# Performance work log

Hardware: AMD Instinct MI355X
Metric: run time of the kernel (lower is better)

Reference implementation:

```python
import jax, jax.numpy as jnp
import numpy as np

T, H, I = 8192, 4096, 11008  # tokens, hidden, intermediate (LLaMA-7B)


def setup_inputs() -> dict:
    key = jax.random.key(0)
    ks = jax.random.split(key, 8)
    # int8-valued tensors stored as int32 (spec dtype enum lacks int8)
    hidden_states = jax.random.randint(ks[0], (T, H), -128, 128, dtype=jnp.int32)
    gate_w = jax.random.randint(ks[1], (I, H), -128, 128, dtype=jnp.int32)
    up_w = jax.random.randint(ks[2], (I, H), -128, 128, dtype=jnp.int32)
    down_w = jax.random.randint(ks[3], (H, I), -128, 128, dtype=jnp.int32)
    # per-tensor dequant scales (alpha = input_scale * weight_scale); small so
    # the SwiGLU product lands roughly in int8 range before requantization
    gate_a = jnp.float32(0.004)
    up_a = jnp.float32(0.004)
    down_a = jnp.float32(0.004)
    gate_b = jax.random.normal(ks[4], (I,), dtype=jnp.float32)
    up_b = jax.random.normal(ks[5], (I,), dtype=jnp.float32)
    down_b = jax.random.normal(ks[6], (H,), dtype=jnp.float32)
    return dict(hidden_states=hidden_states, gate_w=gate_w, gate_a=gate_a,
                gate_b=gate_b, up_w=up_w, up_a=up_a, up_b=up_b,
                down_w=down_w, down_a=down_a, down_b=down_b)


def _w8a8_linear(x_i8, w_i8, alpha, bias):
    # scale alpha and fp32 bias (W8A8BFP32OFP32Linear semantics).
    acc = jnp.matmul(x_i8.astype(jnp.int8), w_i8.astype(jnp.int8).T,
                     preferred_element_type=jnp.int32)
    return acc.astype(jnp.float32) * alpha + bias


def reference(hidden_states, gate_w, gate_a, gate_b, up_w, up_a, up_b,
              down_w, down_a, down_b):
    x1 = jax.nn.silu(_w8a8_linear(hidden_states, gate_w, gate_a, gate_b))  # [T,I]
    x2 = _w8a8_linear(hidden_states, up_w, up_a, up_b)                     # [T,I]
    x = x1 * x2
    # requantize: round, clamp to int8 range
    q = jnp.clip(jnp.round(x), -128.0, 127.0).astype(jnp.int32)
    return _w8a8_linear(q, down_w, down_a, down_b)                          # [T,H]
```

## Files before the change

### kernel.cpp

```cpp
#include <hip/hip_runtime.h>
#include <math.h>

#define T_DIM 8192
#define H_DIM 4096
#define I_DIM 11008

typedef int v4i  __attribute__((ext_vector_type(4)));
typedef int v16i __attribute__((ext_vector_type(16)));

#define MFMA8 __builtin_amdgcn_mfma_i32_32x32x32_i8

#define AS1(p) ((const __attribute__((address_space(1))) void*)(p))
#define AS3(p) ((__attribute__((address_space(3))) void*)(p))

#define WAIT_VM_BAR(N) asm volatile("s_waitcnt vmcnt(" #N ")\n\ts_barrier" ::: "memory")
#define LGKM(N) do { asm volatile("s_waitcnt lgkmcnt(" #N ")" ::: "memory"); \
                     __builtin_amdgcn_sched_barrier(0); } while (0)

__device__ __forceinline__ v4i DSR(const char* p) {
  v4i r;
  unsigned a = (unsigned)(size_t)(const __attribute__((address_space(3))) char*)p;
  asm volatile("ds_read_b128 %0, %1" : "=v"(r) : "v"(a));
  return r;
}

#define STG(buf, src, soff, doff) \
  __builtin_amdgcn_global_load_lds(AS1((src) + (soff)), AS3((buf) + (doff) + dd), 16, 0, 0)

__global__ void pack_shuf(const int* __restrict__ src, char* __restrict__ dst,
                          int nk32, long nchunk) {
  long c = (long)blockIdx.x * blockDim.x + threadIdx.x;
  long stride = (long)gridDim.x * blockDim.x;
  for (; c < nchunk; c += stride) {
    int lane = (int)(c & 63);
    long rk = c >> 6;
    long r32 = rk / nk32;
    int k32 = (int)(rk - r32 * nk32);
    const int4* s = (const int4*)(src + (r32 * 32 + (lane & 31)) * (long)(nk32 * 32)
                                      + (long)k32 * 32 + ((lane >> 5) << 4));
    int4 a = s[0], b = s[1], cc = s[2], d = s[3];
    int w0 = (a.x & 255) | ((a.y & 255) << 8) | ((a.z & 255) << 16) | (a.w << 24);
    int w1 = (b.x & 255) | ((b.y & 255) << 8) | ((b.z & 255) << 16) | (b.w << 24);
    int w2 = (cc.x & 255) | ((cc.y & 255) << 8) | ((cc.z & 255) << 16) | (cc.w << 24);
    int w3 = (d.x & 255) | ((d.y & 255) << 8) | ((d.z & 255) << 16) | (d.w << 24);
    ((int4*)dst)[c] = make_int4(w0, w1, w2, w3);
  }
}

__global__ __launch_bounds__(512, 2) void gemm_gateup(
    const char* __restrict__ A, const char* __restrict__ Bg, const char* __restrict__ Bu,
    const float* __restrict__ ga_p, const float* __restrict__ gb,
    const float* __restrict__ ua_p, const float* __restrict__ ub,
    char* __restrict__ Q)
{
  __shared__ char lds[2][65536];
  const int tid = threadIdx.x;
  const int l = tid & 63;
  const int w = tid >> 6;
  const int wm = w >> 2, wn = w & 3;
  const int li32 = l & 31, kg2 = l >> 5;

  const int q8 = 2752 / 8;
  int bid = blockIdx.x;
  int wgid = (bid & 7) * q8 + (bid >> 3);
  int st = wgid >> 3, r = wgid & 7;
  int sm = st / 43, sn = st - sm * 43;
  const int m0 = (sm * 4 + (r & 3)) * 256;
  const int n0 = (sn * 2 + (r >> 2)) * 128;

  const int NK = H_DIM / 32;
  const int NT = H_DIM / 128;

  v16i accg[4], accu[4];
#pragma unroll
  for (int i = 0; i < 4; ++i) {
#pragma unroll
    for (int j = 0; j < 16; ++j) { accg[i][j] = 0; accu[i][j] = 0; }
  }

  const char* pA = A + ((size_t)((m0 >> 5) + (tid >> 6)) * NK << 10) + ((tid & 63) << 4);
  const char* pB = (tid < 256)
      ? Bg + ((size_t)((n0 >> 5) + (tid >> 6)) * NK << 10) + ((tid & 63) << 4)
      : Bu + ((size_t)((n0 >> 5) + ((tid >> 6) - 4)) * NK << 10) + ((tid & 63) << 4);
  const int dd = tid * 16;

  const int oA0 = (wm * 4 + 0) * 1024 + l * 16;
  const int oA1 = (wm * 4 + 1) * 1024 + l * 16;
  const int oA2 = (wm * 4 + 2) * 1024 + l * 16;
  const int oA3 = (wm * 4 + 3) * 1024 + l * 16;
  const int oG  = 8192  + wn * 1024 + l * 16;
  const int oU  = 12288 + wn * 1024 + l * 16;

  v4i E0, E1, E2, E3, Eg, Eu;
  v4i O0, O1, O2, O3, Og, Ou;

#define RD_GU(S, B, soff)                                                 \
  do {                                                                    \
    S##0 = DSR((B) + (soff) + oA0); S##1 = DSR((B) + (soff) + oA1);       \
    S##2 = DSR((B) + (soff) + oA2); S##3 = DSR((B) + (soff) + oA3);       \
    S##g = DSR((B) + (soff) + oG);  S##u = DSR((B) + (soff) + oU);        \
  } while (0)

#define MM_GU(S)                                                          \
  do {                                                                    \
    __builtin_amdgcn_s_setprio(1);                                        \
    accg[0] = MFMA8(S##0, S##g, accg[0], 0, 0, 0);                        \
    accu[0] = MFMA8(S##0, S##u, accu[0], 0, 0, 0);                        \
    accg[1] = MFMA8(S##1, S##g, accg[1], 0, 0, 0);                        \
    accu[1] = MFMA8(S##1, S##u, accu[1], 0, 0, 0);                        \
    accg[2] = MFMA8(S##2, S##g, accg[2], 0, 0, 0);                        \
    accu[2] = MFMA8(S##2, S##u, accu[2], 0, 0, 0);                        \
    accg[3] = MFMA8(S##3, S##g, accg[3], 0, 0, 0);                        \
    accu[3] = MFMA8(S##3, S##u, accu[3], 0, 0, 0);                        \
    __builtin_amdgcn_s_setprio(0);                                        \
  } while (0)

  {
    char* B0 = lds[0];
    STG(B0, pA, 0,    0);     STG(B0, pA, 1024, 16384);
    STG(B0, pA, 2048, 32768); STG(B0, pA, 3072, 49152);
    STG(B0, pB, 0,    8192);  STG(B0, pB, 1024, 24576);
    STG(B0, pB, 2048, 40960); STG(B0, pB, 3072, 57344);
    WAIT_VM_BAR(0);
    RD_GU(E, B0, 0);
  }

  for (int t = 0; t < NT; ++t) {
    char* L  = lds[t & 1];
    char* SB = lds[(t & 1) ^ 1];
    const bool son = (t + 1) < NT;
    const long sk = (long)(t + 1) * 4096;

    RD_GU(O, L, 16384);
    if (son) { STG(SB, pA, sk, 0);            STG(SB, pA, sk + 1024, 16384);
               STG(SB, pA, sk + 2048, 32768); STG(SB, pA, sk + 3072, 49152); }
    LGKM(6);
    MM_GU(E);
    RD_GU(E, L, 32768);
    if (son) { STG(SB, pB, sk, 8192);         STG(SB, pB, sk + 1024, 24576);
               STG(SB, pB, sk + 2048, 40960); STG(SB, pB, sk + 3072, 57344); }
    LGKM(6);
    MM_GU(O);
    RD_GU(O, L, 49152);
    LGKM(6);
    MM_GU(E);
    LGKM(0);
    MM_GU(O);
    __builtin_amdgcn_sched_barrier(0);
    WAIT_VM_BAR(0);
    if (son) RD_GU(E, SB, 0);
  }
#undef RD_GU
#undef MM_GU

  const float ga = *ga_p, ua = *ua_p;
  const int col = n0 + wn * 32 + li32;
  const float gbv = gb[col], ubv = ub[col];
  const int k32q = (n0 >> 5) + wn;
  const int lanehi = ((li32 >> 4) & 1) << 5;
  const int bytelo = li32 & 15;
  const int NKQ = I_DIM / 32;
#pragma unroll
  for (int mi = 0; mi < 4; ++mi) {
    const int r32q = (m0 >> 5) + wm * 4 + mi;
    char* qbase = Q + ((size_t)(r32q * NKQ + k32q) << 10);
#pragma unroll
    for (int rq = 0; rq < 4; ++rq) {
#pragma unroll
      for (int rr = 0; rr < 4; ++rr) {
        const int rg = rq * 4 + rr;
        const int rowin = kg2 * 4 + rq * 8 + rr;
        float g = (float)accg[mi][rg] * ga + gbv;
        float u = (float)accu[mi][rg] * ua + ubv;
        float x1 = g / (1.0f + expf(-g));
        float x = rintf(x1 * u);
        x = fminf(fmaxf(x, -128.0f), 127.0f);
        qbase[((rowin | lanehi) << 4) + bytelo] = (char)(int)x;
      }
    }
  }
}

__global__ __launch_bounds__(512, 2) void gemm_down(
    const char* __restrict__ Qm, const char* __restrict__ Bd,
    const float* __restrict__ da_p, const float* __restrict__ db,
    float* __restrict__ out)
{
  __shared__ char lds[2][65536];
  const int tid = threadIdx.x;
  const int l = tid & 63;
  const int w = tid >> 6;
  const int wm = w >> 2, wn = w & 3;
  const int li32 = l & 31, kg2 = l >> 5;

  const int q8 = 512 / 8;
  int bid = blockIdx.x;
  int wgid = (bid & 7) * q8 + (bid >> 3);
  int st = wgid >> 3, r = wgid & 7;
  int sm = st >> 3, sn = st & 7;
  const int m0 = (sm * 4 + (r & 3)) * 256;
  const int n0 = (sn * 2 + (r >> 2)) * 256;

  const int NK = I_DIM / 32;
  const int NT = I_DIM / 128;

  v16i acc[4][2];
#pragma unroll
  for (int i = 0; i < 4; ++i) {
#pragma unroll
    for (int n = 0; n < 2; ++n) {
#pragma unroll
      for (int j = 0; j < 16; ++j) acc[i][n][j] = 0;
    }
  }

  const char* pA = Qm + ((size_t)((m0 >> 5) + (tid >> 6)) * NK << 10) + ((tid & 63) << 4);
  const char* pB = Bd + ((size_t)((n0 >> 5) + (tid >> 6)) * NK << 10) + ((tid & 63) << 4);
  const int dd = tid * 16;

  const int oA0 = (wm * 4 + 0) * 1024 + l * 16;
  const int oA1 = (wm * 4 + 1) * 1024 + l * 16;
  const int oA2 = (wm * 4 + 2) * 1024 + l * 16;
  const int oA3 = (wm * 4 + 3) * 1024 + l * 16;
  const int oB0 = 8192 + (wn * 2 + 0) * 1024 + l * 16;
  const int oB1 = 8192 + (wn * 2 + 1) * 1024 + l * 16;

  v4i E0, E1, E2, E3, Eb0, Eb1;
  v4i O0, O1, O2, O3, Ob0, Ob1;

#define RD_DN(S, B, soff)                                                 \
  do {                                                                    \
    S##0 = DSR((B) + (soff) + oA0);  S##1 = DSR((B) + (soff) + oA1);      \
    S##2 = DSR((B) + (soff) + oA2);  S##3 = DSR((B) + (soff) + oA3);      \
    S##b0 = DSR((B) + (soff) + oB0); S##b1 = DSR((B) + (soff) + oB1);     \
  } while (0)

#define MM_DN(S)                                                          \
  do {                                                                    \
    __builtin_amdgcn_s_setprio(1);                                        \
    acc[0][0] = MFMA8(S##0, S##b0, acc[0][0], 0, 0, 0);                   \
    acc[0][1] = MFMA8(S##0, S##b1, acc[0][1], 0, 0, 0);                   \
    acc[1][0] = MFMA8(S##1, S##b0, acc[1][0], 0, 0, 0);                   \
    acc[1][1] = MFMA8(S##1, S##b1, acc[1][1], 0, 0, 0);                   \
    acc[2][0] = MFMA8(S##2, S##b0, acc[2][0], 0, 0, 0);                   \
    acc[2][1] = MFMA8(S##2, S##b1, acc[2][1], 0, 0, 0);                   \
    acc[3][0] = MFMA8(S##3, S##b0, acc[3][0], 0, 0, 0);                   \
    acc[3][1] = MFMA8(S##3, S##b1, acc[3][1], 0, 0, 0);                   \
    __builtin_amdgcn_s_setprio(0);                                        \
  } while (0)

  {
    char* B0 = lds[0];
    STG(B0, pA, 0,    0);     STG(B0, pA, 1024, 16384);
    STG(B0, pA, 2048, 32768); STG(B0, pA, 3072, 49152);
    STG(B0, pB, 0,    8192);  STG(B0, pB, 1024, 24576);
    STG(B0, pB, 2048, 40960); STG(B0, pB, 3072, 57344);
    WAIT_VM_BAR(0);
    RD_DN(E, B0, 0);
  }

  for (int t = 0; t < NT; ++t) {
    char* L  = lds[t & 1];
    char* SB = lds[(t & 1) ^ 1];
    const bool son = (t + 1) < NT;
    const long sk = (long)(t + 1) * 4096;

    RD_DN(O, L, 16384);
    if (son) { STG(SB, pA, sk, 0);            STG(SB, pA, sk + 1024, 16384);
               STG(SB, pA, sk + 2048, 32768); STG(SB, pA, sk + 3072, 49152); }
    LGKM(6);
    MM_DN(E);

    RD_DN(E, L, 32768);
    if (son) { STG(SB, pB, sk, 8192);         STG(SB, pB, sk + 1024, 24576);
               STG(SB, pB, sk + 2048, 40960); STG(SB, pB, sk + 3072, 57344); }
    LGKM(6);
    MM_DN(O);

    RD_DN(O, L, 49152);
    LGKM(6);
    MM_DN(E);

    LGKM(0);
    MM_DN(O);
    __builtin_amdgcn_sched_barrier(0);
    WAIT_VM_BAR(0);
    if (son) RD_DN(E, SB, 0);
  }
#undef RD_DN
#undef MM_DN

  const float da = *da_p;
#pragma unroll
  for (int ni = 0; ni < 2; ++ni) {
    const int col = n0 + wn * 64 + ni * 32 + li32;
    const float dbv = db[col];
#pragma unroll
    for (int mi = 0; mi < 4; ++mi) {
      const int rowb = m0 + wm * 128 + mi * 32 + kg2 * 4;
#pragma unroll
      for (int rq = 0; rq < 4; ++rq) {
#pragma unroll
        for (int rr = 0; rr < 4; ++rr)
          out[(size_t)(rowb + rq * 8 + rr) * H_DIM + col] =
              (float)acc[mi][ni][rq * 4 + rr] * da + dbv;
      }
    }
  }
}

extern "C" void kernel_launch(void* const* d_in, const int* in_sizes, int n_in,
                              void* d_out, int out_size, void* d_ws, size_t ws_size,
                              hipStream_t stream) {
  const int*   hs = (const int*)d_in[0];
  const int*   gw = (const int*)d_in[1];
  const float* ga = (const float*)d_in[2];
  const float* gb = (const float*)d_in[3];
  const int*   uw = (const int*)d_in[4];
  const float* ua = (const float*)d_in[5];
  const float* ub = (const float*)d_in[6];
  const int*   dw = (const int*)d_in[7];
  const float* da = (const float*)d_in[8];
  const float* db = (const float*)d_in[9];

  char* ws   = (char*)d_ws;
  char* hidS = ws;
  char* gS   = hidS + (size_t)T_DIM * H_DIM;
  char* uS   = gS   + (size_t)I_DIM * H_DIM;
  char* dS   = uS   + (size_t)I_DIM * H_DIM;
  char* qS   = dS   + (size_t)H_DIM * I_DIM;

  pack_shuf<<<2048, 256, 0, stream>>>(hs, hidS, H_DIM / 32, (long)T_DIM * H_DIM / 16);
  pack_shuf<<<2048, 256, 0, stream>>>(gw, gS,   H_DIM / 32, (long)I_DIM * H_DIM / 16);
  pack_shuf<<<2048, 256, 0, stream>>>(uw, uS,   H_DIM / 32, (long)I_DIM * H_DIM / 16);
  pack_shuf<<<2048, 256, 0, stream>>>(dw, dS,   I_DIM / 32, (long)H_DIM * I_DIM / 16);

  gemm_gateup<<<2752, 512, 0, stream>>>(hidS, gS, uS, ga, gb, ua, ub, qS);
  gemm_down<<<512, 512, 0, stream>>>(qS, dS, da, db, (float*)d_out);
}
```

Before: 1.151 ms.

## Halve workgroup to 4 waves, doubling per-wave MFMA tile in both GEMMs

Both GEMM kernels drop from 512 to 256 threads per block while keeping the same block tile, so each wave now computes twice as many 32x32 output tiles (8 accumulators per gate/up, 16 in down). Each staging step issues twice as many global-to-LDS loads per thread, and LDS read counts per wave grow to 8. The aim is better reuse of operand registers per MFMA and fewer LDS reads per MFMA. The cost is much higher accumulator register pressure, which likely limits occupancy to one block per CU, giving less latency hiding.

```diff
diff --git a/kernel.cpp b/kernel.cpp
--- a/kernel.cpp
+++ b/kernel.cpp
@@ -47,7 +47,7 @@
   }
 }
 
-__global__ __launch_bounds__(512, 2) void gemm_gateup(
+__global__ __launch_bounds__(256, 1) void gemm_gateup(
     const char* __restrict__ A, const char* __restrict__ Bg, const char* __restrict__ Bu,
     const float* __restrict__ ga_p, const float* __restrict__ gb,
     const float* __restrict__ ua_p, const float* __restrict__ ub,
@@ -57,7 +57,7 @@
   const int tid = threadIdx.x;
   const int l = tid & 63;
   const int w = tid >> 6;
-  const int wm = w >> 2, wn = w & 3;
+  const int wm = w >> 1, wn = w & 1;
   const int li32 = l & 31, kg2 = l >> 5;
 
   const int q8 = 2752 / 8;
@@ -71,56 +71,90 @@
   const int NK = H_DIM / 32;
   const int NT = H_DIM / 128;
 
-  v16i accg[4], accu[4];
-#pragma unroll
-  for (int i = 0; i < 4; ++i) {
-#pragma unroll
-    for (int j = 0; j < 16; ++j) { accg[i][j] = 0; accu[i][j] = 0; }
-  }
-
-  const char* pA = A + ((size_t)((m0 >> 5) + (tid >> 6)) * NK << 10) + ((tid & 63) << 4);
-  const char* pB = (tid < 256)
-      ? Bg + ((size_t)((n0 >> 5) + (tid >> 6)) * NK << 10) + ((tid & 63) << 4)
-      : Bu + ((size_t)((n0 >> 5) + ((tid >> 6) - 4)) * NK << 10) + ((tid & 63) << 4);
+  v16i accg[4][2], accu[4][2];
+#pragma unroll
+  for (int i = 0; i < 4; ++i)
+#pragma unroll
+    for (int n = 0; n < 2; ++n)
+#pragma unroll
+      for (int j = 0; j < 16; ++j) { accg[i][n][j] = 0; accu[i][n][j] = 0; }
+
+  const int tf = tid >> 6, tl = (tid & 63) << 4;
+  const char* pA0 = A  + ((size_t)((m0 >> 5) + tf)     * NK << 10) + tl;
+  const char* pA1 = A  + ((size_t)((m0 >> 5) + 4 + tf) * NK << 10) + tl;
+  const char* pG  = Bg + ((size_t)((n0 >> 5) + tf)     * NK << 10) + tl;
+  const char* pU  = Bu + ((size_t)((n0 >> 5) + tf)     * NK << 10) + tl;
   const int dd = tid * 16;
 
-  const int oA0 = (wm * 4 + 0) * 1024 + l * 16;
-  const int oA1 = (wm * 4 + 1) * 1024 + l * 16;
-  const int oA2 = (wm * 4 + 2) * 1024 + l * 16;
-  const int oA3 = (wm * 4 + 3) * 1024 + l * 16;
-  const int oG  = 8192  + wn * 1024 + l * 16;
-  const int oU  = 12288 + wn * 1024 + l * 16;
-
-  v4i E0, E1, E2, E3, Eg, Eu;
-  v4i O0, O1, O2, O3, Og, Ou;
+  const int lo = l * 16;
+  const int oA0 = (wm * 4 + 0) * 1024 + lo;
+  const int oA1 = (wm * 4 + 1) * 1024 + lo;
+  const int oA2 = (wm * 4 + 2) * 1024 + lo;
+  const int oA3 = (wm * 4 + 3) * 1024 + lo;
+  const int oG0 = 8192  + (wn * 2 + 0) * 1024 + lo;
+  const int oG1 = 8192  + (wn * 2 + 1) * 1024 + lo;
+  const int oU0 = 12288 + (wn * 2 + 0) * 1024 + lo;
+  const int oU1 = 12288 + (wn * 2 + 1) * 1024 + lo;
+
+  v4i E0, E1, E2, E3, Eg0, Eg1, Eu0, Eu1;
+  v4i O0, O1, O2, O3, Og0, Og1, Ou0, Ou1;
 
 #define RD_GU(S, B, soff)                                                 \
   do {                                                                    \
-    S##0 = DSR((B) + (soff) + oA0); S##1 = DSR((B) + (soff) + oA1);       \
-    S##2 = DSR((B) + (soff) + oA2); S##3 = DSR((B) + (soff) + oA3);       \
-    S##g = DSR((B) + (soff) + oG);  S##u = DSR((B) + (soff) + oU);        \
+    S##0 = DSR((B) + (soff) + oA0);  S##1 = DSR((B) + (soff) + oA1);      \
+    S##2 = DSR((B) + (soff) + oA2);  S##3 = DSR((B) + (soff) + oA3);      \
+    S##g0 = DSR((B) + (soff) + oG0); S##g1 = DSR((B) + (soff) + oG1);     \
+    S##u0 = DSR((B) + (soff) + oU0); S##u1 = DSR((B) + (soff) + oU1);     \
   } while (0)
 
 #define MM_GU(S)                                                          \
   do {                                                                    \
     __builtin_amdgcn_s_setprio(1);                                        \
-    accg[0] = MFMA8(S##0, S##g, accg[0], 0, 0, 0);                        \
-    accu[0] = MFMA8(S##0, S##u, accu[0], 0, 0, 0);                        \
-    accg[1] = MFMA8(S##1, S##g, accg[1], 0, 0, 0);                        \
-    accu[1] = MFMA8(S##1, S##u, accu[1], 0, 0, 0);                        \
-    accg[2] = MFMA8(S##2, S##g, accg[2], 0, 0, 0);                        \
-    accu[2] = MFMA8(S##2, S##u, accu[2], 0, 0, 0);                        \
-    accg[3] = MFMA8(S##3, S##g, accg[3], 0, 0, 0);                        \
-    accu[3] = MFMA8(S##3, S##u, accu[3], 0, 0, 0);                        \
+    accg[0][0] = MFMA8(S##0, S##g0, accg[0][0], 0, 0, 0);                 \
+    accg[0][1] = MFMA8(S##0, S##g1, accg[0][1], 0, 0, 0);                 \
+    accu[0][0] = MFMA8(S##0, S##u0, accu[0][0], 0, 0, 0);                 \
+    accu[0][1] = MFMA8(S##0, S##u1, accu[0][1], 0, 0, 0);                 \
+    accg[1][0] = MFMA8(S##1, S##g0, accg[1][0], 0, 0, 0);                 \
+    accg[1][1] = MFMA8(S##1, S##g1, accg[1][1], 0, 0, 0);                 \
+    accu[1][0] = MFMA8(S##1, S##u0, accu[1][0], 0, 0, 0);                 \
+    accu[1][1] = MFMA8(S##1, S##u1, accu[1][1], 0, 0, 0);                 \
+    accg[2][0] = MFMA8(S##2, S##g0, accg[2][0], 0, 0, 0);                 \
+    accg[2][1] = MFMA8(S##2, S##g1, accg[2][1], 0, 0, 0);                 \
+    accu[2][0] = MFMA8(S##2, S##u0, accu[2][0], 0, 0, 0);                 \
+    accu[2][1] = MFMA8(S##2, S##u1, accu[2][1], 0, 0, 0);                 \
+    accg[3][0] = MFMA8(S##3, S##g0, accg[3][0], 0, 0, 0);                 \
+    accg[3][1] = MFMA8(S##3, S##g1, accg[3][1], 0, 0, 0);                 \
+    accu[3][0] = MFMA8(S##3, S##u0, accu[3][0], 0, 0, 0);                 \
+    accu[3][1] = MFMA8(S##3, S##u1, accu[3][1], 0, 0, 0);                 \
     __builtin_amdgcn_s_setprio(0);                                        \
+  } while (0)
+
+#define STAGE_GU(B, kb)                                                   \
+  do {                                                                    \
+    STG(B, pA0, ((kb) + 0) * 1024, 0);                                    \
+    STG(B, pA1, ((kb) + 0) * 1024, 4096);                                 \
+    STG(B, pG,  ((kb) + 0) * 1024, 8192);                                 \
+    STG(B, pU,  ((kb) + 0) * 1024, 12288);                                \
+    STG(B, pA0, ((kb) + 1) * 1024, 16384);                                \
+    STG(B, pA1, ((kb) + 1) * 1024, 20480);                                \
+    STG(B, pG,  ((kb) + 1) * 1024, 24576);                                \
+    STG(B, pU,  ((kb) + 1) * 1024, 28672);                                \
+  } while (0)
+#define STAGE_GU2(B, kb)                                                  \
+  do {                                                                    \
+    STG(B, pA0, ((kb) + 2) * 1024, 32768);                                \
+    STG(B, pA1, ((kb) + 2) * 1024, 36864);                                \
+    STG(B, pG,  ((kb) + 2) * 1024, 40960);                                \
+    STG(B, pU,  ((kb) + 2) * 1024, 45056);                                \
+    STG(B, pA0, ((kb) + 3) * 1024, 49152);                                \
+    STG(B, pA1, ((kb) + 3) * 1024, 53248);                                \
+    STG(B, pG,  ((kb) + 3) * 1024, 57344);                                \
+    STG(B, pU,  ((kb) + 3) * 1024, 61440);                                \
   } while (0)
 
   {
     char* B0 = lds[0];
-    STG(B0, pA, 0,    0);     STG(B0, pA, 1024, 16384);
-    STG(B0, pA, 2048, 32768); STG(B0, pA, 3072, 49152);
-    STG(B0, pB, 0,    8192);  STG(B0, pB, 1024, 24576);
-    STG(B0, pB, 2048, 40960); STG(B0, pB, 3072, 57344);
+    STAGE_GU(B0, 0); STAGE_GU2(B0, 0);
     WAIT_VM_BAR(0);
     RD_GU(E, B0, 0);
   }
@@ -129,20 +163,18 @@
     char* L  = lds[t & 1];
     char* SB = lds[(t & 1) ^ 1];
     const bool son = (t + 1) < NT;
-    const long sk = (long)(t + 1) * 4096;
+    const int kb = (t + 1) * 4;
 
     RD_GU(O, L, 16384);
-    if (son) { STG(SB, pA, sk, 0);            STG(SB, pA, sk + 1024, 16384);
-               STG(SB, pA, sk + 2048, 32768); STG(SB, pA, sk + 3072, 49152); }
-    LGKM(6);
+    if (son) STAGE_GU(SB, kb);
+    LGKM(8);
     MM_GU(E);
     RD_GU(E, L, 32768);
-    if (son) { STG(SB, pB, sk, 8192);         STG(SB, pB, sk + 1024, 24576);
-               STG(SB, pB, sk + 2048, 40960); STG(SB, pB, sk + 3072, 57344); }
-    LGKM(6);
+    if (son) STAGE_GU2(SB, kb);
+    LGKM(8);
     MM_GU(O);
     RD_GU(O, L, 49152);
-    LGKM(6);
+    LGKM(8);
     MM_GU(E);
     LGKM(0);
     MM_GU(O);
@@ -152,36 +184,41 @@
   }
 #undef RD_GU
 #undef MM_GU
+#undef STAGE_GU
+#undef STAGE_GU2
 
   const float ga = *ga_p, ua = *ua_p;
-  const int col = n0 + wn * 32 + li32;
-  const float gbv = gb[col], ubv = ub[col];
-  const int k32q = (n0 >> 5) + wn;
   const int lanehi = ((li32 >> 4) & 1) << 5;
   const int bytelo = li32 & 15;
   const int NKQ = I_DIM / 32;
 #pragma unroll
-  for (int mi = 0; mi < 4; ++mi) {
-    const int r32q = (m0 >> 5) + wm * 4 + mi;
-    char* qbase = Q + ((size_t)(r32q * NKQ + k32q) << 10);
-#pragma unroll
-    for (int rq = 0; rq < 4; ++rq) {
-#pragma unroll
-      for (int rr = 0; rr < 4; ++rr) {
-        const int rg = rq * 4 + rr;
-        const int rowin = kg2 * 4 + rq * 8 + rr;
-        float g = (float)accg[mi][rg] * ga + gbv;
-        float u = (float)accu[mi][rg] * ua + ubv;
-        float x1 = g / (1.0f + expf(-g));
-        float x = rintf(x1 * u);
-        x = fminf(fmaxf(x, -128.0f), 127.0f);
-        qbase[((rowin | lanehi) << 4) + bytelo] = (char)(int)x;
+  for (int ni = 0; ni < 2; ++ni) {
+    const int col = n0 + wn * 64 + ni * 32 + li32;
+    const float gbv = gb[col], ubv = ub[col];
+    const int k32q = (n0 >> 5) + wn * 2 + ni;
+#pragma unroll
+    for (int mi = 0; mi < 4; ++mi) {
+      const int r32q = (m0 >> 5) + wm * 4 + mi;
+      char* qbase = Q + ((size_t)(r32q * NKQ + k32q) << 10);
+#pragma unroll
+      for (int rq = 0; rq < 4; ++rq) {
+#pragma unroll
+        for (int rr = 0; rr < 4; ++rr) {
+          const int rg = rq * 4 + rr;
+          const int rowin = kg2 * 4 + rq * 8 + rr;
+          float g = (float)accg[mi][ni][rg] * ga + gbv;
+          float u = (float)accu[mi][ni][rg] * ua + ubv;
+          float x1 = g / (1.0f + expf(-g));
+          float x = rintf(x1 * u);
+          x = fminf(fmaxf(x, -128.0f), 127.0f);
+          qbase[((rowin | lanehi) << 4) + bytelo] = (char)(int)x;
+        }
       }
     }
   }
 }
 
-__global__ __launch_bounds__(512, 2) void gemm_down(
+__global__ __launch_bounds__(256, 1) void gemm_down(
     const char* __restrict__ Qm, const char* __restrict__ Bd,
     const float* __restrict__ da_p, const float* __restrict__ db,
     float* __restrict__ out)
@@ -190,7 +227,7 @@
   const int tid = threadIdx.x;
   const int l = tid & 63;
   const int w = tid >> 6;
-  const int wm = w >> 2, wn = w & 3;
+  const int wm = w >> 1, wn = w & 1;
   const int li32 = l & 31, kg2 = l >> 5;
 
   const int q8 = 512 / 8;
@@ -204,35 +241,40 @@
   const int NK = I_DIM / 32;
   const int NT = I_DIM / 128;
 
-  v16i acc[4][2];
-#pragma unroll
-  for (int i = 0; i < 4; ++i) {
-#pragma unroll
-    for (int n = 0; n < 2; ++n) {
+  v16i acc[4][4];
+#pragma unroll
+  for (int i = 0; i < 4; ++i)
+#pragma unroll
+    for (int n = 0; n < 4; ++n)
 #pragma unroll
       for (int j = 0; j < 16; ++j) acc[i][n][j] = 0;
-    }
-  }
-
-  const char* pA = Qm + ((size_t)((m0 >> 5) + (tid >> 6)) * NK << 10) + ((tid & 63) << 4);
-  const char* pB = Bd + ((size_t)((n0 >> 5) + (tid >> 6)) * NK << 10) + ((tid & 63) << 4);
+
+  const int tf = tid >> 6, tl = (tid & 63) << 4;
+  const char* pA0 = Qm + ((size_t)((m0 >> 5) + tf)     * NK << 10) + tl;
+  const char* pA1 = Qm + ((size_t)((m0 >> 5) + 4 + tf) * NK << 10) + tl;
+  const char* pB0 = Bd + ((size_t)((n0 >> 5) + tf)     * NK << 10) + tl;
+  const char* pB1 = Bd + ((size_t)((n0 >> 5) + 4 + tf) * NK << 10) + tl;
   const int dd = tid * 16;
 
-  const int oA0 = (wm * 4 + 0) * 1024 + l * 16;
-  const int oA1 = (wm * 4 + 1) * 1024 + l * 16;
-  const int oA2 = (wm * 4 + 2) * 1024 + l * 16;
-  const int oA3 = (wm * 4 + 3) * 1024 + l * 16;
-  const int oB0 = 8192 + (wn * 2 + 0) * 1024 + l * 16;
-  const int oB1 = 8192 + (wn * 2 + 1) * 1024 + l * 16;
-
-  v4i E0, E1, E2, E3, Eb0, Eb1;
-  v4i O0, O1, O2, O3, Ob0, Ob1;
+  const int lo = l * 16;
+  const int oA0 = (wm * 4 + 0) * 1024 + lo;
+  const int oA1 = (wm * 4 + 1) * 1024 + lo;
+  const int oA2 = (wm * 4 + 2) * 1024 + lo;
+  const int oA3 = (wm * 4 + 3) * 1024 + lo;
+  const int oB0 = 8192 + (wn * 4 + 0) * 1024 + lo;
+  const int oB1 = 8192 + (wn * 4 + 1) * 1024 + lo;
+  const int oB2 = 8192 + (wn * 4 + 2) * 1024 + lo;
+  const int oB3 = 8192 + (wn * 4 + 3) * 1024 + lo;
+
+  v4i E0, E1, E2, E3, Eb0, Eb1, Eb2, Eb3;
+  v4i O0, O1, O2, O3, Ob0, Ob1, Ob2, Ob3;
 
 #define RD_DN(S, B, soff)                                                 \
   do {                                                                    \
     S##0 = DSR((B) + (soff) + oA0);  S##1 = DSR((B) + (soff) + oA1);      \
     S##2 = DSR((B) + (soff) + oA2);  S##3 = DSR((B) + (soff) + oA3);      \
     S##b0 = DSR((B) + (soff) + oB0); S##b1 = DSR((B) + (soff) + oB1);     \
+    S##b2 = DSR((B) + (soff) + oB2); S##b3 = DSR((B) + (soff) + oB3);     \
   } while (0)
 
 #define MM_DN(S)                                                          \
@@ -240,21 +282,49 @@
     __builtin_amdgcn_s_setprio(1);                                        \
     acc[0][0] = MFMA8(S##0, S##b0, acc[0][0], 0, 0, 0);                   \
     acc[0][1] = MFMA8(S##0, S##b1, acc[0][1], 0, 0, 0);                   \
+    acc[0][2] = MFMA8(S##0, S##b2, acc[0][2], 0, 0, 0);                   \
+    acc[0][3] = MFMA8(S##0, S##b3, acc[0][3], 0, 0, 0);                   \
     acc[1][0] = MFMA8(S##1, S##b0, acc[1][0], 0, 0, 0);                   \
     acc[1][1] = MFMA8(S##1, S##b1, acc[1][1], 0, 0, 0);                   \
+    acc[1][2] = MFMA8(S##1, S##b2, acc[1][2], 0, 0, 0);                   \
+    acc[1][3] = MFMA8(S##1, S##b3, acc[1][3], 0, 0, 0);                   \
     acc[2][0] = MFMA8(S##2, S##b0, acc[2][0], 0, 0, 0);                   \
     acc[2][1] = MFMA8(S##2, S##b1, acc[2][1], 0, 0, 0);                   \
+    acc[2][2] = MFMA8(S##2, S##b2, acc[2][2], 0, 0, 0);                   \
+    acc[2][3] = MFMA8(S##2, S##b3, acc[2][3], 0, 0, 0);                   \
     acc[3][0] = MFMA8(S##3, S##b0, acc[3][0], 0, 0, 0);                   \
     acc[3][1] = MFMA8(S##3, S##b1, acc[3][1], 0, 0, 0);                   \
+    acc[3][2] = MFMA8(S##3, S##b2, acc[3][2], 0, 0, 0);                   \
+    acc[3][3] = MFMA8(S##3, S##b3, acc[3][3], 0, 0, 0);                   \
     __builtin_amdgcn_s_setprio(0);                                        \
+  } while (0)
+
+#define STAGE_DN(B, kb)                                                   \
+  do {                                                                    \
+    STG(B, pA0, ((kb) + 0) * 1024, 0);                                    \
+    STG(B, pA1, ((kb) + 0) * 1024, 4096);                                 \
+    STG(B, pB0, ((kb) + 0) * 1024, 8192);                                 \
+    STG(B, pB1, ((kb) + 0) * 1024, 12288);                                \
+    STG(B, pA0, ((kb) + 1) * 1024, 16384);                                \
+    STG(B, pA1, ((kb) + 1) * 1024, 20480);                                \
+    STG(B, pB0, ((kb) + 1) * 1024, 24576);                                \
+    STG(B, pB1, ((kb) + 1) * 1024, 28672);                                \
+  } while (0)
+#define STAGE_DN2(B, kb)                                                  \
+  do {                                                                    \
+    STG(B, pA0, ((kb) + 2) * 1024, 32768);                                \
+    STG(B, pA1, ((kb) + 2) * 1024, 36864);                                \
+    STG(B, pB0, ((kb) + 2) * 1024, 40960);                                \
+    STG(B, pB1, ((kb) + 2) * 1024, 45056);                                \
+    STG(B, pA0, ((kb) + 3) * 1024, 49152);                                \
+    STG(B, pA1, ((kb) + 3) * 1024, 53248);                                \
+    STG(B, pB0, ((kb) + 3) * 1024, 57344);                                \
+    STG(B, pB1, ((kb) + 3) * 1024, 61440);                                \
   } while (0)
 
   {
     char* B0 = lds[0];
-    STG(B0, pA, 0,    0);     STG(B0, pA, 1024, 16384);
-    STG(B0, pA, 2048, 32768); STG(B0, pA, 3072, 49152);
-    STG(B0, pB, 0,    8192);  STG(B0, pB, 1024, 24576);
-    STG(B0, pB, 2048, 40960); STG(B0, pB, 3072, 57344);
+    STAGE_DN(B0, 0); STAGE_DN2(B0, 0);
     WAIT_VM_BAR(0);
     RD_DN(E, B0, 0);
   }
@@ -263,22 +333,20 @@
     char* L  = lds[t & 1];
     char* SB = lds[(t & 1) ^ 1];
     const bool son = (t + 1) < NT;
-    const long sk = (long)(t + 1) * 4096;
+    const int kb = (t + 1) * 4;
 
     RD_DN(O, L, 16384);
-    if (son) { STG(SB, pA, sk, 0);            STG(SB, pA, sk + 1024, 16384);
-               STG(SB, pA, sk + 2048, 32768); STG(SB, pA, sk + 3072, 49152); }
-    LGKM(6);
+    if (son) STAGE_DN(SB, kb);
+    LGKM(8);
     MM_DN(E);
 
     RD_DN(E, L, 32768);
-    if (son) { STG(SB, pB, sk, 8192);         STG(SB, pB, sk + 1024, 24576);
-               STG(SB, pB, sk + 2048, 40960); STG(SB, pB, sk + 3072, 57344); }
-    LGKM(6);
+    if (son) STAGE_DN2(SB, kb);
+    LGKM(8);
     MM_DN(O);
 
     RD_DN(O, L, 49152);
-    LGKM(6);
+    LGKM(8);
     MM_DN(E);
 
     LGKM(0);
@@ -289,11 +357,13 @@
   }
 #undef RD_DN
 #undef MM_DN
+#undef STAGE_DN
+#undef STAGE_DN2
 
   const float da = *da_p;
 #pragma unroll
-  for (int ni = 0; ni < 2; ++ni) {
-    const int col = n0 + wn * 64 + ni * 32 + li32;
+  for (int ni = 0; ni < 4; ++ni) {
+    const int col = n0 + wn * 128 + ni * 32 + li32;
     const float dbv = db[col];
 #pragma unroll
     for (int mi = 0; mi < 4; ++mi) {
@@ -335,6 +405,6 @@
   pack_shuf<<<2048, 256, 0, stream>>>(uw, uS,   H_DIM / 32, (long)I_DIM * H_DIM / 16);
   pack_shuf<<<2048, 256, 0, stream>>>(dw, dS,   I_DIM / 32, (long)H_DIM * I_DIM / 16);
 
-  gemm_gateup<<<2752, 512, 0, stream>>>(hidS, gS, uS, ga, gb, ua, ub, qS);
-  gemm_down<<<512, 512, 0, stream>>>(qS, dS, da, db, (float*)d_out);
+  gemm_gateup<<<2752, 256, 0, stream>>>(hidS, gS, uS, ga, gb, ua, ub, qS);
+  gemm_down<<<512, 256, 0, stream>>>(qS, dS, da, db, (float*)d_out);
 }
```

New measurement: 1.164 ms. About the same (+1.1%).

## Switch GEMM K-loop to three-stage LDS ring with half-size K tiles

Applied to the files above, without the earlier changes.

Both int8 GEMM kernels move from a double-buffered 128-deep K tile (64KB per stage) to a triple-buffered 64-deep K tile (32KB per stage), rotating three LDS buffers. Loads for tile t+2 are issued while tile t is computed, and the wait drops from vmcnt(0) to vmcnt(4), so one stage of global loads stays in flight across the barrier. The aim is to hide global-load latency and reduce the full drain at each iteration. In exchange there are twice as many iterations and barriers, and the clamped tail re-stages the last tile.

```diff
diff --git a/kernel.cpp b/kernel.cpp
--- a/kernel.cpp
+++ b/kernel.cpp
@@ -13,7 +13,9 @@
 #define AS1(p) ((const __attribute__((address_space(1))) void*)(p))
 #define AS3(p) ((__attribute__((address_space(3))) void*)(p))
 
-#define WAIT_VM_BAR(N) asm volatile("s_waitcnt vmcnt(" #N ")\n\ts_barrier" ::: "memory")
+#define WAITV(N) do { asm volatile("s_waitcnt vmcnt(" #N ")" ::: "memory"); \
+                      __builtin_amdgcn_sched_barrier(0); } while (0)
+#define BAR() __builtin_amdgcn_s_barrier()
 #define LGKM(N) do { asm volatile("s_waitcnt lgkmcnt(" #N ")" ::: "memory"); \
                      __builtin_amdgcn_sched_barrier(0); } while (0)
 
@@ -24,8 +26,8 @@
   return r;
 }
 
-#define STG(buf, src, soff, doff) \
-  __builtin_amdgcn_global_load_lds(AS1((src) + (soff)), AS3((buf) + (doff) + dd), 16, 0, 0)
+#define STG(ldst, gsrc) \
+  __builtin_amdgcn_global_load_lds(AS1(gsrc), AS3(ldst), 16, 0, 0)
 
 __global__ void pack_shuf(const int* __restrict__ src, char* __restrict__ dst,
                           int nk32, long nchunk) {
@@ -53,7 +55,7 @@
     const float* __restrict__ ua_p, const float* __restrict__ ub,
     char* __restrict__ Q)
 {
-  __shared__ char lds[2][65536];
+  __shared__ char lds[3][32768];
   const int tid = threadIdx.x;
   const int l = tid & 63;
   const int w = tid >> 6;
@@ -69,36 +71,51 @@
   const int n0 = (sn * 2 + (r >> 2)) * 128;
 
   const int NK = H_DIM / 32;
-  const int NT = H_DIM / 128;
+  const int NT = H_DIM / 64;
 
   v16i accg[4], accu[4];
 #pragma unroll
-  for (int i = 0; i < 4; ++i) {
+  for (int i = 0; i < 4; ++i)
 #pragma unroll
     for (int j = 0; j < 16; ++j) { accg[i][j] = 0; accu[i][j] = 0; }
-  }
-
-  const char* pA = A + ((size_t)((m0 >> 5) + (tid >> 6)) * NK << 10) + ((tid & 63) << 4);
-  const char* pB = (tid < 256)
-      ? Bg + ((size_t)((n0 >> 5) + (tid >> 6)) * NK << 10) + ((tid & 63) << 4)
-      : Bu + ((size_t)((n0 >> 5) + ((tid >> 6) - 4)) * NK << 10) + ((tid & 63) << 4);
-  const int dd = tid * 16;
-
-  const int oA0 = (wm * 4 + 0) * 1024 + l * 16;
-  const int oA1 = (wm * 4 + 1) * 1024 + l * 16;
-  const int oA2 = (wm * 4 + 2) * 1024 + l * 16;
-  const int oA3 = (wm * 4 + 3) * 1024 + l * 16;
-  const int oG  = 8192  + wn * 1024 + l * 16;
-  const int oU  = 12288 + wn * 1024 + l * 16;
+
+  const int lo = l * 16;
+  const char* pA0 = A  + ((size_t)((m0 >> 5) + w) * NK + 0) * 1024 + lo;
+  const char* pA1 = A  + ((size_t)((m0 >> 5) + w) * NK + 1) * 1024 + lo;
+  const char* pG  = Bg + ((size_t)((n0 >> 5) + (w >> 1)) * NK + (w & 1)) * 1024 + lo;
+  const char* pU  = Bu + ((size_t)((n0 >> 5) + (w >> 1)) * NK + (w & 1)) * 1024 + lo;
+  const int dA0 = w * 2048 + lo;
+  const int dA1 = dA0 + 1024;
+  const int dG  = 16384 + w * 1024 + lo;
+  const int dU  = dG + 8192;
+
+#define STAGE_GU(SB, tt)                                                  \
+  do {                                                                    \
+    size_t so = (size_t)(tt) * 2048;                                      \
+    STG((SB) + dA0, pA0 + so);                                            \
+    STG((SB) + dA1, pA1 + so);                                            \
+    STG((SB) + dG,  pG  + so);                                            \
+    STG((SB) + dU,  pU  + so);                                            \
+  } while (0)
+
+  const int oA0 = (wm * 4 + 0) * 2048 + lo;
+  const int oA1 = (wm * 4 + 1) * 2048 + lo;
+  const int oA2 = (wm * 4 + 2) * 2048 + lo;
+  const int oA3 = (wm * 4 + 3) * 2048 + lo;
+  const int oG  = 16384 + wn * 2048 + lo;
+  const int oU  = 24576 + wn * 2048 + lo;
 
   v4i E0, E1, E2, E3, Eg, Eu;
   v4i O0, O1, O2, O3, Og, Ou;
 
-#define RD_GU(S, B, soff)                                                 \
-  do {                                                                    \
-    S##0 = DSR((B) + (soff) + oA0); S##1 = DSR((B) + (soff) + oA1);       \
-    S##2 = DSR((B) + (soff) + oA2); S##3 = DSR((B) + (soff) + oA3);       \
-    S##g = DSR((B) + (soff) + oG);  S##u = DSR((B) + (soff) + oU);        \
+#define RD_GU(S, B, s)                                                    \
+  do {                                                                    \
+    S##0 = DSR((B) + oA0 + (s) * 1024);                                   \
+    S##1 = DSR((B) + oA1 + (s) * 1024);                                   \
+    S##2 = DSR((B) + oA2 + (s) * 1024);                                   \
+    S##3 = DSR((B) + oA3 + (s) * 1024);                                   \
+    S##g = DSR((B) + oG  + (s) * 1024);                                   \
+    S##u = DSR((B) + oU  + (s) * 1024);                                   \
   } while (0)
 
 #define MM_GU(S)                                                          \
@@ -115,43 +132,39 @@
     __builtin_amdgcn_s_setprio(0);                                        \
   } while (0)
 
+  char* b0 = lds[0];
+  char* b1 = lds[1];
+  char* b2 = lds[2];
+
   {
-    char* B0 = lds[0];
-    STG(B0, pA, 0,    0);     STG(B0, pA, 1024, 16384);
-    STG(B0, pA, 2048, 32768); STG(B0, pA, 3072, 49152);
-    STG(B0, pB, 0,    8192);  STG(B0, pB, 1024, 24576);
-    STG(B0, pB, 2048, 40960); STG(B0, pB, 3072, 57344);
-    WAIT_VM_BAR(0);
-    RD_GU(E, B0, 0);
+    STAGE_GU(b0, 0);
+    STAGE_GU(b1, 1);
+    WAITV(4);
+    BAR();
+    RD_GU(E, b0, 0);
   }
 
   for (int t = 0; t < NT; ++t) {
-    char* L  = lds[t & 1];
-    char* SB = lds[(t & 1) ^ 1];
-    const bool son = (t + 1) < NT;
-    const long sk = (long)(t + 1) * 4096;
-
-    RD_GU(O, L, 16384);
-    if (son) { STG(SB, pA, sk, 0);            STG(SB, pA, sk + 1024, 16384);
-               STG(SB, pA, sk + 2048, 32768); STG(SB, pA, sk + 3072, 49152); }
+    const int tstage = (t + 2 < NT) ? (t + 2) : (NT - 1);
+    RD_GU(O, b0, 1);
+    STAGE_GU(b2, tstage);
     LGKM(6);
     MM_GU(E);
-    RD_GU(E, L, 32768);
-    if (son) { STG(SB, pB, sk, 8192);         STG(SB, pB, sk + 1024, 24576);
-               STG(SB, pB, sk + 2048, 40960); STG(SB, pB, sk + 3072, 57344); }
-    LGKM(6);
+    WAITV(4);
+    BAR();
+    if (t + 1 < NT) {
+      RD_GU(E, b1, 0);
+      LGKM(6);
+    } else {
+      LGKM(0);
+    }
     MM_GU(O);
-    RD_GU(O, L, 49152);
-    LGKM(6);
-    MM_GU(E);
-    LGKM(0);
-    MM_GU(O);
-    __builtin_amdgcn_sched_barrier(0);
-    WAIT_VM_BAR(0);
-    if (son) RD_GU(E, SB, 0);
-  }
+    char* tmp = b0; b0 = b1; b1 = b2; b2 = tmp;
+  }
+  WAITV(0);
 #undef RD_GU
 #undef MM_GU
+#undef STAGE_GU
 
   const float ga = *ga_p, ua = *ua_p;
   const int col = n0 + wn * 32 + li32;
@@ -186,7 +199,7 @@
     const float* __restrict__ da_p, const float* __restrict__ db,
     float* __restrict__ out)
 {
-  __shared__ char lds[2][65536];
+  __shared__ char lds[3][32768];
   const int tid = threadIdx.x;
   const int l = tid & 63;
   const int w = tid >> 6;
@@ -202,37 +215,53 @@
   const int n0 = (sn * 2 + (r >> 2)) * 256;
 
   const int NK = I_DIM / 32;
-  const int NT = I_DIM / 128;
+  const int NT = I_DIM / 64;
 
   v16i acc[4][2];
 #pragma unroll
-  for (int i = 0; i < 4; ++i) {
-#pragma unroll
-    for (int n = 0; n < 2; ++n) {
+  for (int i = 0; i < 4; ++i)
+#pragma unroll
+    for (int n = 0; n < 2; ++n)
 #pragma unroll
       for (int j = 0; j < 16; ++j) acc[i][n][j] = 0;
-    }
-  }
-
-  const char* pA = Qm + ((size_t)((m0 >> 5) + (tid >> 6)) * NK << 10) + ((tid & 63) << 4);
-  const char* pB = Bd + ((size_t)((n0 >> 5) + (tid >> 6)) * NK << 10) + ((tid & 63) << 4);
-  const int dd = tid * 16;
-
-  const int oA0 = (wm * 4 + 0) * 1024 + l * 16;
-  const int oA1 = (wm * 4 + 1) * 1024 + l * 16;
-  const int oA2 = (wm * 4 + 2) * 1024 + l * 16;
-  const int oA3 = (wm * 4 + 3) * 1024 + l * 16;
-  const int oB0 = 8192 + (wn * 2 + 0) * 1024 + l * 16;
-  const int oB1 = 8192 + (wn * 2 + 1) * 1024 + l * 16;
+
+  const int lo = l * 16;
+  const char* pA0 = Qm + ((size_t)((m0 >> 5) + w) * NK + 0) * 1024 + lo;
+  const char* pA1 = Qm + ((size_t)((m0 >> 5) + w) * NK + 1) * 1024 + lo;
+  const char* pB0 = Bd + ((size_t)((n0 >> 5) + w) * NK + 0) * 1024 + lo;
+  const char* pB1 = Bd + ((size_t)((n0 >> 5) + w) * NK + 1) * 1024 + lo;
+  const int dA0 = w * 2048 + lo;
+  const int dA1 = dA0 + 1024;
+  const int dB0 = 16384 + w * 2048 + lo;
+  const int dB1 = dB0 + 1024;
+
+#define STAGE_DN(SB, tt)                                                  \
+  do {                                                                    \
+    size_t so = (size_t)(tt) * 2048;                                      \
+    STG((SB) + dA0, pA0 + so);                                            \
+    STG((SB) + dA1, pA1 + so);                                            \
+    STG((SB) + dB0, pB0 + so);                                            \
+    STG((SB) + dB1, pB1 + so);                                            \
+  } while (0)
+
+  const int oA0 = (wm * 4 + 0) * 2048 + lo;
+  const int oA1 = (wm * 4 + 1) * 2048 + lo;
+  const int oA2 = (wm * 4 + 2) * 2048 + lo;
+  const int oA3 = (wm * 4 + 3) * 2048 + lo;
+  const int oB0 = 16384 + (wn * 2 + 0) * 2048 + lo;
+  const int oB1 = 16384 + (wn * 2 + 1) * 2048 + lo;
 
   v4i E0, E1, E2, E3, Eb0, Eb1;
   v4i O0, O1, O2, O3, Ob0, Ob1;
 
-#define RD_DN(S, B, soff)                                                 \
-  do {                                                                    \
-    S##0 = DSR((B) + (soff) + oA0);  S##1 = DSR((B) + (soff) + oA1);      \
-    S##2 = DSR((B) + (soff) + oA2);  S##3 = DSR((B) + (soff) + oA3);      \
-    S##b0 = DSR((B) + (soff) + oB0); S##b1 = DSR((B) + (soff) + oB1);     \
+#define RD_DN(S, B, s)                                                    \
+  do {                                                                    \
+    S##0 = DSR((B) + oA0 + (s) * 1024);                                   \
+    S##1 = DSR((B) + oA1 + (s) * 1024);                                   \
+    S##2 = DSR((B) + oA2 + (s) * 1024);                                   \
+    S##3 = DSR((B) + oA3 + (s) * 1024);                                   \
+    S##b0 = DSR((B) + oB0 + (s) * 1024);                                  \
+    S##b1 = DSR((B) + oB1 + (s) * 1024);                                  \
   } while (0)
 
 #define MM_DN(S)                                                          \
@@ -249,46 +278,41 @@
     __builtin_amdgcn_s_setprio(0);                                        \
   } while (0)
 
+  char* b0 = lds[0];
+  char* b1 = lds[1];
+  char* b2 = lds[2];
+
   {
-    char* B0 = lds[0];
-    STG(B0, pA, 0,    0);     STG(B0, pA, 1024, 16384);
-    STG(B0, pA, 2048, 32768); STG(B0, pA, 3072, 49152);
-    STG(B0, pB, 0,    8192);  STG(B0, pB, 1024, 24576);
-    STG(B0, pB, 2048, 40960); STG(B0, pB, 3072, 57344);
-    WAIT_VM_BAR(0);
-    RD_DN(E, B0, 0);
+    STAGE_DN(b0, 0);
+    STAGE_DN(b1, 1);
+    WAITV(4);
+    BAR();
+    RD_DN(E, b0, 0);
   }
 
   for (int t = 0; t < NT; ++t) {
-    char* L  = lds[t & 1];
-    char* SB = lds[(t & 1) ^ 1];
-    const bool son = (t + 1) < NT;
-    const long sk = (long)(t + 1) * 4096;
-
-    RD_DN(O, L, 16384);
-    if (son) { STG(SB, pA, sk, 0);            STG(SB, pA, sk + 1024, 16384);
-               STG(SB, pA, sk + 2048, 32768); STG(SB, pA, sk + 3072, 49152); }
+    const int tstage = (t + 2 < NT) ? (t + 2) : (NT - 1);
+    RD_DN(O, b0, 1);
+    STAGE_DN(b2, tstage);
     LGKM(6);
     MM_DN(E);
 
-    RD_DN(E, L, 32768);
-    if (son) { STG(SB, pB, sk, 8192);         STG(SB, pB, sk + 1024, 24576);
-               STG(SB, pB, sk + 2048, 40960); STG(SB, pB, sk + 3072, 57344); }
-    LGKM(6);
+    WAITV(4);
+    BAR();
+    if (t + 1 < NT) {
+      RD_DN(E, b1, 0);
+      LGKM(6);
+    } else {
+      LGKM(0);
+    }
     MM_DN(O);
 
-    RD_DN(O, L, 49152);
-    LGKM(6);
-    MM_DN(E);
-
-    LGKM(0);
-    MM_DN(O);
-    __builtin_amdgcn_sched_barrier(0);
-    WAIT_VM_BAR(0);
-    if (son) RD_DN(E, SB, 0);
-  }
+    char* tmp = b0; b0 = b1; b1 = b2; b2 = tmp;
+  }
+  WAITV(0);
 #undef RD_DN
 #undef MM_DN
+#undef STAGE_DN
 
   const float da = *da_p;
 #pragma unroll
```

New measurement: 1.089 ms. -5.3%, faster.
